# Optimization experiments

Measured on AMD Instinct MI355X. Metric: run time of the kernel, lower is better.

## Reference

```python
import jax, jax.numpy as jnp
import numpy as np

N_A = 100000   # target-type nodes
N_B = 100000   # source-type nodes
IN_DIM = 256
OUT_DIM = 256
E = 320000     # edges per meta-path
LN_EPS = 1e-5


def setup_inputs() -> dict:
    key = jax.random.key(0)
    ks = jax.random.split(key, 10)
    w_scale = 1.0 / np.sqrt(IN_DIM)
    return {
        "x_A": jax.random.normal(ks[0], (N_A, IN_DIM), jnp.float32),
        "x_B": jax.random.normal(ks[1], (N_B, IN_DIM), jnp.float32),
        "edge_index0": jax.random.randint(ks[2], (2, E), 0, N_A, dtype=jnp.int32),
        "edge_index1": jax.random.randint(ks[3], (2, E), 0, N_A, dtype=jnp.int32),
        "W0": jax.random.normal(ks[4], (IN_DIM, OUT_DIM), jnp.float32) * w_scale,
        "b0": jnp.zeros((OUT_DIM,), jnp.float32),
        "W1": jax.random.normal(ks[5], (IN_DIM, OUT_DIM), jnp.float32) * w_scale,
        "b1": jnp.zeros((OUT_DIM,), jnp.float32),
        "sem_vec": jax.random.normal(ks[6], (OUT_DIM,), jnp.float32),
        "gamma": jnp.ones((OUT_DIM,), jnp.float32),
        "beta": jnp.zeros((OUT_DIM,), jnp.float32),
    }


def _layer_norm(x, gamma, beta):
    mu = jnp.mean(x, axis=-1, keepdims=True)
    var = jnp.mean((x - mu) ** 2, axis=-1, keepdims=True)
    return (x - mu) * jax.lax.rsqrt(var + LN_EPS) * gamma + beta


def _path_mean_agg(x_src, W, b, ei, n_dst):
    # project ALL source nodes first (matches torch: proj_src = Linear(src_x))
    proj = x_src @ W + b                      # (N_src, OUT)
    msgs = proj[ei[0]]                        # gather  (E, OUT)
    agg = jax.ops.segment_sum(msgs, ei[1], num_segments=n_dst)   # scatter_add
    cnt = jax.ops.segment_sum(jnp.ones((ei.shape[1],), proj.dtype), ei[1],
                              num_segments=n_dst)
    return agg / jnp.clip(cnt, 1.0)[:, None]  # count-normalized mean


def reference(x_A, x_B, edge_index0, edge_index1, W0, b0, W1, b1,
              sem_vec, gamma, beta):
    n_dst = x_A.shape[0]
    agg0 = _path_mean_agg(x_B, W0, b0, edge_index0, n_dst)
    agg1 = _path_mean_agg(x_B, W1, b1, edge_index1, n_dst)
    stack = jnp.stack([agg0, agg1], axis=0)               # (P=2, N_A, OUT)
    scores = jnp.einsum('pnd,d->pn', jnp.tanh(stack), sem_vec)
    weights = jax.nn.softmax(scores, axis=0)              # over meta-paths
    fused = jnp.sum(stack * weights[..., None], axis=0)   # (N_A, OUT)
    out_A = _layer_norm(jax.nn.relu(fused), gamma, beta)
    out_B = jnp.zeros((x_B.shape[0], OUT_DIM), x_B.dtype)  # no path targets B
    return out_A, out_B
```

## Files before the change

kernel.cpp:

```cpp
#include <hip/hip_runtime.h>
#include <math.h>

#define NA 100000
#define NB 100000
#define KDIM 256
#define ODIM 256
#define NEDGE 320000
#define CAP 32
#define NBUCK (2 * NA)

typedef unsigned int u32;
typedef _Float16 f16x8 __attribute__((ext_vector_type(8)));
typedef float    f32x4 __attribute__((ext_vector_type(4)));

__global__ __launch_bounds__(256) void convert_w(
    const float* __restrict__ W0, const float* __restrict__ b0,
    const float* __restrict__ W1, const float* __restrict__ b1,
    _Float16* __restrict__ Wth, float* __restrict__ bcat)
{
    const int t = blockIdx.x * 256 + threadIdx.x;
    if (t >= 512 * 32) return;
    const int n  = t >> 5;
    const int kb = (t & 31) * 8;
    const float* src = (n < ODIM) ? (W0 + n) : (W1 + (n - ODIM));
    f16x8 vh;
    #pragma unroll
    for (int j = 0; j < 8; ++j)
        vh[j] = (_Float16)src[(size_t)(kb + j) * ODIM];
    *(f16x8*)&Wth[(size_t)n * KDIM + kb] = vh;
    if ((t & 31) == 0) bcat[n] = (n < ODIM) ? b0[n] : b1[n - ODIM];
}

__global__ __launch_bounds__(256) void convert_x(
    const float* __restrict__ x, _Float16* __restrict__ xh)
{
    const size_t c = ((size_t)blockIdx.x * 256 + threadIdx.x) * 8;
    const float4* p = (const float4*)&x[c];
    float4 a = p[0], b = p[1];
    f16x8 v;
    v[0] = (_Float16)a.x; v[1] = (_Float16)a.y;
    v[2] = (_Float16)a.z; v[3] = (_Float16)a.w;
    v[4] = (_Float16)b.x; v[5] = (_Float16)b.y;
    v[6] = (_Float16)b.z; v[7] = (_Float16)b.w;
    *(f16x8*)&xh[c] = v;
}

__global__ __launch_bounds__(256) void bucket_fill(
    const int* __restrict__ ei0, const int* __restrict__ ei1,
    u32* __restrict__ cnt, int* __restrict__ elist)
{
    const int gid = blockIdx.x * 256 + threadIdx.x;
    if (gid >= 2 * NEDGE) return;
    const int p = (gid >= NEDGE) ? 1 : 0;
    const int j = gid - p * NEDGE;
    const int* ei = p ? ei1 : ei0;
    const int src = ei[j];
    const int dst = ei[NEDGE + j];
    const u32 b = (u32)(p * NA + dst);
    const u32 pos = atomicAdd(&cnt[b], 1u);
    if (pos < CAP) elist[(size_t)b * CAP + pos] = src;
}

__global__ __launch_bounds__(256) void agg_mean(
    const _Float16* __restrict__ xh, const u32* __restrict__ cnt,
    const int* __restrict__ elist, _Float16* __restrict__ aggx)
{
    const int row  = (int)((blockIdx.x * (size_t)blockDim.x + threadIdx.x) >> 6);
    const int lane = threadIdx.x & 63;
    if (row >= NA) return;
    const int p  = lane >> 5;
    const int li = lane & 31;
    const int c  = li * 8;

    const u32 b  = (u32)(p * NA + row);
    const u32 nt = cnt[b];
    const u32 n  = min(nt, (u32)CAP);
    const int* el = &elist[(size_t)b * CAP];

    float a[8] = {};
    for (u32 j = 0; j < n; ++j) {
        const int src = el[j];
        const f16x8 v = *(const f16x8*)&xh[(size_t)src * KDIM + c];
        #pragma unroll
        for (int i = 0; i < 8; ++i) a[i] += (float)v[i];
    }
    const float inv = 1.0f / fmaxf((float)nt, 1.0f);
    f16x8 o;
    #pragma unroll
    for (int i = 0; i < 8; ++i) o[i] = (_Float16)(a[i] * inv);
    *(f16x8*)&aggx[((size_t)p * NA + row) * KDIM + c] = o;
}

__global__ __launch_bounds__(256) void proj_gemm(
    const _Float16* __restrict__ aggx, const _Float16* __restrict__ Wth,
    const float* __restrict__ bcat, _Float16* __restrict__ pagg)
{
    __shared__ __align__(16) char smem[17408];
    f16x8* Ah = (f16x8*)smem;
    f16x8* Bh = (f16x8*)(smem + 8192);

    const int t    = threadIdx.x;
    const int w    = t >> 6;
    const int lane = t & 63;
    const int p    = (blockIdx.y >= 782) ? 1 : 0;
    const int m0   = (blockIdx.y - p * 782) * 128;
    const int n0   = blockIdx.x * 128;
    const int wm   = w & 1, wn = w >> 1;
    const int r16  = lane & 15;
    const int kc   = (lane >> 4) * 8;
    const int srow = w * 16 + r16;

    const int arow0 = min(m0 + srow,      NA - 1);
    const int arow1 = min(m0 + srow + 64, NA - 1);
    const _Float16* Ap = aggx + (size_t)p * NA * KDIM;
    const int brow0 = p * 256 + n0 + srow;
    const int brow1 = brow0 + 64;

    f32x4 acc[4][4] = {};

    for (int k0 = 0; k0 < KDIM; k0 += 32) {
        f16x8 ga0 = *(const f16x8*)&Ap[(size_t)arow0 * KDIM + k0 + kc];
        f16x8 ga1 = *(const f16x8*)&Ap[(size_t)arow1 * KDIM + k0 + kc];
        f16x8 gh0 = *(const f16x8*)&Wth[(size_t)brow0 * KDIM + k0 + kc];
        f16x8 gh1 = *(const f16x8*)&Wth[(size_t)brow1 * KDIM + k0 + kc];

        __syncthreads();
        Ah[t] = ga0;  Ah[t + 256] = ga1;
        Bh[t] = gh0;  Bh[t + 256] = gh1;
        __syncthreads();

        f16x8 af[4], bgh[4];
        #pragma unroll
        for (int i = 0; i < 4; ++i) af[i] = Ah[(wm * 4 + i) * 64 + lane];
        #pragma unroll
        for (int j = 0; j < 4; ++j) bgh[j] = Bh[(wn * 4 + j) * 64 + lane];
        #pragma unroll
        for (int i = 0; i < 4; ++i)
            #pragma unroll
            for (int j = 0; j < 4; ++j)
                acc[i][j] = __builtin_amdgcn_mfma_f32_16x16x32_f16(
                    af[i], bgh[j], acc[i][j], 0, 0, 0);
    }

    float bias[4];
    #pragma unroll
    for (int j = 0; j < 4; ++j)
        bias[j] = bcat[p * 256 + n0 + wn * 64 + j * 16 + r16];

    const int quad = lane >> 4, c16 = lane & 15;
    const int lr = lane >> 2, lc = (lane & 3) * 16;

    for (int i = 0; i < 4; ++i) {
        __syncthreads();
        float* ep = (float*)(smem + w * 4352);
        #pragma unroll
        for (int j = 0; j < 4; ++j)
            #pragma unroll
            for (int r = 0; r < 4; ++r)
                ep[(quad * 4 + r) * 68 + j * 16 + c16] = acc[i][j][r] + bias[j];
        __syncthreads();
        f32x4 v0 = *(f32x4*)&ep[lr * 68 + lc + 0];
        f32x4 v1 = *(f32x4*)&ep[lr * 68 + lc + 4];
        f32x4 v2 = *(f32x4*)&ep[lr * 68 + lc + 8];
        f32x4 v3 = *(f32x4*)&ep[lr * 68 + lc + 12];
        const int rg = m0 + wm * 64 + i * 16 + lr;
        if (rg < NA) {
            f16x8 o0, o1;
            o0[0] = (_Float16)v0[0]; o0[1] = (_Float16)v0[1];
            o0[2] = (_Float16)v0[2]; o0[3] = (_Float16)v0[3];
            o0[4] = (_Float16)v1[0]; o0[5] = (_Float16)v1[1];
            o0[6] = (_Float16)v1[2]; o0[7] = (_Float16)v1[3];
            o1[0] = (_Float16)v2[0]; o1[1] = (_Float16)v2[1];
            o1[2] = (_Float16)v2[2]; o1[3] = (_Float16)v2[3];
            o1[4] = (_Float16)v3[0]; o1[5] = (_Float16)v3[1];
            o1[6] = (_Float16)v3[2]; o1[7] = (_Float16)v3[3];
            _Float16* dst = &pagg[((size_t)p * NA + rg) * ODIM + n0 + wn * 64 + lc];
            *(f16x8*)(dst + 0) = o0;
            *(f16x8*)(dst + 8) = o1;
        }
    }
}

__global__ __launch_bounds__(256) void finalize(
    _Float16* __restrict__ pagg, const u32* __restrict__ cnt,
    float* __restrict__ out,
    const float* __restrict__ sem, const float* __restrict__ gamma,
    const float* __restrict__ beta)
{
    const int row  = (int)((blockIdx.x * (size_t)blockDim.x + threadIdx.x) >> 6);
    const int lane = threadIdx.x & 63;
    if (row >= NA) return;
    const int p  = lane >> 5;
    const int li = lane & 31;
    const int c  = li * 8;

    const u32 n = cnt[p * NA + row];
    _Float16* pp = &pagg[((size_t)p * NA + row) * ODIM + c];
    const f16x8 v = *(const f16x8*)pp;
    float m[8];
    #pragma unroll
    for (int i = 0; i < 8; ++i) m[i] = (n > 0) ? (float)v[i] : 0.0f;

    f16x8 z = {};
    *(f16x8*)pp = z;

    float4 s0 = *(const float4*)&sem[c];
    float4 s1 = *(const float4*)&sem[c + 4];
    float sv[8] = {s0.x, s0.y, s0.z, s0.w, s1.x, s1.y, s1.z, s1.w};
    float s = 0.f;
    #pragma unroll
    for (int i = 0; i < 8; ++i) s += tanhf(m[i]) * sv[i];
    #pragma unroll
    for (int off = 1; off <= 16; off <<= 1) s += __shfl_xor(s, off);
    const float so = __shfl_xor(s, 32);
    const float mx = fmaxf(s, so);
    const float e  = __expf(s - mx), eo = __expf(so - mx);
    const float wown = e / (e + eo), woth = eo / (e + eo);

    float fused[8];
    float sum = 0.f, sq = 0.f;
    #pragma unroll
    for (int i = 0; i < 8; ++i) {
        const float mo = __shfl_xor(m[i], 32);
        float f = fmaxf(wown * m[i] + woth * mo, 0.f);
        fused[i] = f;
        sum += f;
        sq  += f * f;
    }
    #pragma unroll
    for (int off = 1; off <= 32; off <<= 1) {
        sum += __shfl_xor(sum, off);
        sq  += __shfl_xor(sq,  off);
    }
    const float mu  = sum * (0.5f / ODIM);
    const float var = sq  * (0.5f / ODIM) - mu * mu;
    const float rinv = rsqrtf(var + 1e-5f);

    if (p == 0) {
        float4 g0 = *(const float4*)&gamma[c];
        float4 g1 = *(const float4*)&gamma[c + 4];
        float4 b0 = *(const float4*)&beta[c];
        float4 b1 = *(const float4*)&beta[c + 4];
        float gv[8] = {g0.x, g0.y, g0.z, g0.w, g1.x, g1.y, g1.z, g1.w};
        float bv[8] = {b0.x, b0.y, b0.z, b0.w, b1.x, b1.y, b1.z, b1.w};
        float o[8];
        #pragma unroll
        for (int i = 0; i < 8; ++i) o[i] = (fused[i] - mu) * rinv * gv[i] + bv[i];
        float4 o0, o1;
        o0.x = o[0]; o0.y = o[1]; o0.z = o[2]; o0.w = o[3];
        o1.x = o[4]; o1.y = o[5]; o1.z = o[6]; o1.w = o[7];
        *(float4*)&out[(size_t)row * ODIM + c]     = o0;
        *(float4*)&out[(size_t)row * ODIM + c + 4] = o1;
    }
}

extern "C" void kernel_launch(void* const* d_in, const int* in_sizes, int n_in,
                              void* d_out, int out_size, void* d_ws, size_t ws_size,
                              hipStream_t stream)
{
    const float* xB   = (const float*)d_in[1];
    const int*   ei0  = (const int*)d_in[2];
    const int*   ei1  = (const int*)d_in[3];
    const float* W0   = (const float*)d_in[4];
    const float* b0   = (const float*)d_in[5];
    const float* W1   = (const float*)d_in[6];
    const float* b1   = (const float*)d_in[7];
    const float* sem  = (const float*)d_in[8];
    const float* gam  = (const float*)d_in[9];
    const float* bet  = (const float*)d_in[10];

    float* out = (float*)d_out;

    _Float16* xh   = (_Float16*)d_ws;
    _Float16* aggx = xh + (size_t)NB * KDIM;
    u32* cnt   = (u32*)(aggx + (size_t)2 * NA * KDIM);
    int* elist = (int*)(cnt + NBUCK);
    _Float16* Wth = (_Float16*)(elist + (size_t)NBUCK * CAP);
    float*    bcat = (float*)(Wth + (size_t)512 * KDIM);

    _Float16* pagg = (_Float16*)(out + (size_t)NA * ODIM);

    convert_w<<<64, 256, 0, stream>>>(W0, b0, W1, b1, Wth, bcat);

    convert_x<<<(NB * KDIM / 8) / 256, 256, 0, stream>>>(xB, xh);

    hipMemsetAsync(cnt, 0, (size_t)NBUCK * sizeof(u32), stream);
    bucket_fill<<<(2 * NEDGE + 255) / 256, 256, 0, stream>>>(ei0, ei1, cnt, elist);

    agg_mean<<<(NA + 3) / 4, 256, 0, stream>>>(xh, cnt, elist, aggx);

    proj_gemm<<<dim3(2, 1564), 256, 0, stream>>>(aggx, Wth, bcat, pagg);

    finalize<<<(NA + 3) / 4, 256, 0, stream>>>(pagg, cnt, out, sem, gam, bet);
}
```

Measured before the change: 582.6 us.

## Fuse projection GEMM with semantic-attention and LayerNorm finalize via shared memory

Merges the projection GEMM and the finalize kernel into one kernel. Each block computes a 64-row tile for both meta-paths, keeps the fp16 projected results in LDS, and runs softmax fusion and LayerNorm from there. This removes the round trip of the intermediate projected tensor through global memory (previously staged in out_B) and one launch. The same kernel now zeroes out_B directly. In exchange, B fragments are read straight from global memory rather than shared, the accumulator count per thread doubles (register pressure), and the large LDS buffer may lower occupancy.

```diff
diff --git a/kernel.cpp b/kernel.cpp
--- a/kernel.cpp
+++ b/kernel.cpp
@@ -91,166 +91,147 @@
     *(f16x8*)&aggx[((size_t)p * NA + row) * KDIM + c] = o;
 }
 
-__global__ __launch_bounds__(256) void proj_gemm(
+__global__ __launch_bounds__(256) void gemm_finalize(
     const _Float16* __restrict__ aggx, const _Float16* __restrict__ Wth,
-    const float* __restrict__ bcat, _Float16* __restrict__ pagg)
-{
-    __shared__ __align__(16) char smem[17408];
-    f16x8* Ah = (f16x8*)smem;
-    f16x8* Bh = (f16x8*)(smem + 8192);
+    const float* __restrict__ bcat, const u32* __restrict__ cnt,
+    const float* __restrict__ sem, const float* __restrict__ gamma,
+    const float* __restrict__ beta, float* __restrict__ out)
+{
+    __shared__ __align__(16) f16x8 Ah[512];
+    __shared__ __align__(16) _Float16 P[64][520];
 
     const int t    = threadIdx.x;
     const int w    = t >> 6;
     const int lane = t & 63;
-    const int p    = (blockIdx.y >= 782) ? 1 : 0;
-    const int m0   = (blockIdx.y - p * 782) * 128;
-    const int n0   = blockIdx.x * 128;
-    const int wm   = w & 1, wn = w >> 1;
+    const int m0   = blockIdx.x * 64;
+    const int p    = w >> 1;
+    const int n0w  = (w & 1) * 128;
     const int r16  = lane & 15;
     const int kc   = (lane >> 4) * 8;
     const int srow = w * 16 + r16;
 
-    const int arow0 = min(m0 + srow,      NA - 1);
-    const int arow1 = min(m0 + srow + 64, NA - 1);
-    const _Float16* Ap = aggx + (size_t)p * NA * KDIM;
-    const int brow0 = p * 256 + n0 + srow;
-    const int brow1 = brow0 + 64;
-
-    f32x4 acc[4][4] = {};
+    {
+        float* outB = out + (size_t)NA * ODIM;
+        f32x4 z = {};
+        #pragma unroll
+        for (int it = 0; it < 16; ++it) {
+            const int idx = it * 256 + t;
+            const int r = idx >> 6;
+            if (m0 + r < NA)
+                *(f32x4*)&outB[(size_t)(m0 + r) * ODIM + (idx & 63) * 4] = z;
+        }
+    }
+
+    const int arow  = min(m0 + srow, NA - 1);
+    const size_t a0off = (size_t)arow * KDIM + kc;
+    const size_t a1off = ((size_t)NA + arow) * KDIM + kc;
+
+    int boff[8];
+    #pragma unroll
+    for (int j = 0; j < 8; ++j)
+        boff[j] = (p * 256 + n0w + j * 16 + r16) * KDIM + kc;
+
+    f32x4 acc[4][8] = {};
 
     for (int k0 = 0; k0 < KDIM; k0 += 32) {
-        f16x8 ga0 = *(const f16x8*)&Ap[(size_t)arow0 * KDIM + k0 + kc];
-        f16x8 ga1 = *(const f16x8*)&Ap[(size_t)arow1 * KDIM + k0 + kc];
-        f16x8 gh0 = *(const f16x8*)&Wth[(size_t)brow0 * KDIM + k0 + kc];
-        f16x8 gh1 = *(const f16x8*)&Wth[(size_t)brow1 * KDIM + k0 + kc];
-
+        const f16x8 ga0 = *(const f16x8*)&aggx[a0off + k0];
+        const f16x8 ga1 = *(const f16x8*)&aggx[a1off + k0];
         __syncthreads();
         Ah[t] = ga0;  Ah[t + 256] = ga1;
-        Bh[t] = gh0;  Bh[t + 256] = gh1;
         __syncthreads();
 
-        f16x8 af[4], bgh[4];
-        #pragma unroll
-        for (int i = 0; i < 4; ++i) af[i] = Ah[(wm * 4 + i) * 64 + lane];
-        #pragma unroll
-        for (int j = 0; j < 4; ++j) bgh[j] = Bh[(wn * 4 + j) * 64 + lane];
-        #pragma unroll
-        for (int i = 0; i < 4; ++i)
+        f16x8 af[4];
+        #pragma unroll
+        for (int i = 0; i < 4; ++i) af[i] = Ah[p * 256 + i * 64 + lane];
+        #pragma unroll
+        for (int j = 0; j < 8; ++j) {
+            const f16x8 bh = *(const f16x8*)&Wth[boff[j] + k0];
             #pragma unroll
-            for (int j = 0; j < 4; ++j)
+            for (int i = 0; i < 4; ++i)
                 acc[i][j] = __builtin_amdgcn_mfma_f32_16x16x32_f16(
-                    af[i], bgh[j], acc[i][j], 0, 0, 0);
-    }
-
-    float bias[4];
-    #pragma unroll
-    for (int j = 0; j < 4; ++j)
-        bias[j] = bcat[p * 256 + n0 + wn * 64 + j * 16 + r16];
+                    af[i], bh, acc[i][j], 0, 0, 0);
+        }
+    }
 
     const int quad = lane >> 4, c16 = lane & 15;
-    const int lr = lane >> 2, lc = (lane & 3) * 16;
-
-    for (int i = 0; i < 4; ++i) {
-        __syncthreads();
-        float* ep = (float*)(smem + w * 4352);
-        #pragma unroll
-        for (int j = 0; j < 4; ++j)
+    float bias[8];
+    #pragma unroll
+    for (int j = 0; j < 8; ++j)
+        bias[j] = bcat[p * 256 + n0w + j * 16 + c16];
+    #pragma unroll
+    for (int i = 0; i < 4; ++i)
+        #pragma unroll
+        for (int j = 0; j < 8; ++j)
             #pragma unroll
-            for (int r = 0; r < 4; ++r)
-                ep[(quad * 4 + r) * 68 + j * 16 + c16] = acc[i][j][r] + bias[j];
-        __syncthreads();
-        f32x4 v0 = *(f32x4*)&ep[lr * 68 + lc + 0];
-        f32x4 v1 = *(f32x4*)&ep[lr * 68 + lc + 4];
-        f32x4 v2 = *(f32x4*)&ep[lr * 68 + lc + 8];
-        f32x4 v3 = *(f32x4*)&ep[lr * 68 + lc + 12];
-        const int rg = m0 + wm * 64 + i * 16 + lr;
-        if (rg < NA) {
-            f16x8 o0, o1;
-            o0[0] = (_Float16)v0[0]; o0[1] = (_Float16)v0[1];
-            o0[2] = (_Float16)v0[2]; o0[3] = (_Float16)v0[3];
-            o0[4] = (_Float16)v1[0]; o0[5] = (_Float16)v1[1];
-            o0[6] = (_Float16)v1[2]; o0[7] = (_Float16)v1[3];
-            o1[0] = (_Float16)v2[0]; o1[1] = (_Float16)v2[1];
-            o1[2] = (_Float16)v2[2]; o1[3] = (_Float16)v2[3];
-            o1[4] = (_Float16)v3[0]; o1[5] = (_Float16)v3[1];
-            o1[6] = (_Float16)v3[2]; o1[7] = (_Float16)v3[3];
-            _Float16* dst = &pagg[((size_t)p * NA + rg) * ODIM + n0 + wn * 64 + lc];
-            *(f16x8*)(dst + 0) = o0;
-            *(f16x8*)(dst + 8) = o1;
-        }
-    }
-}
-
-__global__ __launch_bounds__(256) void finalize(
-    _Float16* __restrict__ pagg, const u32* __restrict__ cnt,
-    float* __restrict__ out,
-    const float* __restrict__ sem, const float* __restrict__ gamma,
-    const float* __restrict__ beta)
-{
-    const int row  = (int)((blockIdx.x * (size_t)blockDim.x + threadIdx.x) >> 6);
-    const int lane = threadIdx.x & 63;
-    if (row >= NA) return;
-    const int p  = lane >> 5;
+            for (int e = 0; e < 4; ++e)
+                P[i * 16 + quad * 4 + e][p * 256 + n0w + j * 16 + c16] =
+                    (_Float16)(acc[i][j][e] + bias[j]);
+    __syncthreads();
+
+    const int fp = lane >> 5;
     const int li = lane & 31;
     const int c  = li * 8;
 
-    const u32 n = cnt[p * NA + row];
-    _Float16* pp = &pagg[((size_t)p * NA + row) * ODIM + c];
-    const f16x8 v = *(const f16x8*)pp;
-    float m[8];
-    #pragma unroll
-    for (int i = 0; i < 8; ++i) m[i] = (n > 0) ? (float)v[i] : 0.0f;
-
-    f16x8 z = {};
-    *(f16x8*)pp = z;
-
-    float4 s0 = *(const float4*)&sem[c];
-    float4 s1 = *(const float4*)&sem[c + 4];
-    float sv[8] = {s0.x, s0.y, s0.z, s0.w, s1.x, s1.y, s1.z, s1.w};
-    float s = 0.f;
-    #pragma unroll
-    for (int i = 0; i < 8; ++i) s += tanhf(m[i]) * sv[i];
-    #pragma unroll
-    for (int off = 1; off <= 16; off <<= 1) s += __shfl_xor(s, off);
-    const float so = __shfl_xor(s, 32);
-    const float mx = fmaxf(s, so);
-    const float e  = __expf(s - mx), eo = __expf(so - mx);
-    const float wown = e / (e + eo), woth = eo / (e + eo);
-
-    float fused[8];
-    float sum = 0.f, sq = 0.f;
-    #pragma unroll
-    for (int i = 0; i < 8; ++i) {
-        const float mo = __shfl_xor(m[i], 32);
-        float f = fmaxf(wown * m[i] + woth * mo, 0.f);
-        fused[i] = f;
-        sum += f;
-        sq  += f * f;
-    }
-    #pragma unroll
-    for (int off = 1; off <= 32; off <<= 1) {
-        sum += __shfl_xor(sum, off);
-        sq  += __shfl_xor(sq,  off);
-    }
-    const float mu  = sum * (0.5f / ODIM);
-    const float var = sq  * (0.5f / ODIM) - mu * mu;
-    const float rinv = rsqrtf(var + 1e-5f);
-
-    if (p == 0) {
-        float4 g0 = *(const float4*)&gamma[c];
-        float4 g1 = *(const float4*)&gamma[c + 4];
-        float4 b0 = *(const float4*)&beta[c];
-        float4 b1 = *(const float4*)&beta[c + 4];
-        float gv[8] = {g0.x, g0.y, g0.z, g0.w, g1.x, g1.y, g1.z, g1.w};
-        float bv[8] = {b0.x, b0.y, b0.z, b0.w, b1.x, b1.y, b1.z, b1.w};
-        float o[8];
-        #pragma unroll
-        for (int i = 0; i < 8; ++i) o[i] = (fused[i] - mu) * rinv * gv[i] + bv[i];
-        float4 o0, o1;
-        o0.x = o[0]; o0.y = o[1]; o0.z = o[2]; o0.w = o[3];
-        o1.x = o[4]; o1.y = o[5]; o1.z = o[6]; o1.w = o[7];
-        *(float4*)&out[(size_t)row * ODIM + c]     = o0;
-        *(float4*)&out[(size_t)row * ODIM + c + 4] = o1;
+    for (int rr = 0; rr < 16; ++rr) {
+        const int r  = w * 16 + rr;
+        const int rg = m0 + r;
+        if (rg >= NA) break;
+
+        const u32 n = cnt[fp * NA + rg];
+        const f16x8 v = *(const f16x8*)&P[r][fp * 256 + c];
+        float m[8];
+        #pragma unroll
+        for (int i = 0; i < 8; ++i) m[i] = (n > 0) ? (float)v[i] : 0.0f;
+
+        float4 s0 = *(const float4*)&sem[c];
+        float4 s1 = *(const float4*)&sem[c + 4];
+        float sv[8] = {s0.x, s0.y, s0.z, s0.w, s1.x, s1.y, s1.z, s1.w};
+        float s = 0.f;
+        #pragma unroll
+        for (int i = 0; i < 8; ++i) s += tanhf(m[i]) * sv[i];
+        #pragma unroll
+        for (int off = 1; off <= 16; off <<= 1) s += __shfl_xor(s, off);
+        const float so = __shfl_xor(s, 32);
+        const float mx = fmaxf(s, so);
+        const float e  = __expf(s - mx), eo = __expf(so - mx);
+        const float wown = e / (e + eo), woth = eo / (e + eo);
+
+        float fused[8];
+        float sum = 0.f, sq = 0.f;
+        #pragma unroll
+        for (int i = 0; i < 8; ++i) {
+            const float mo = __shfl_xor(m[i], 32);
+            float f = fmaxf(wown * m[i] + woth * mo, 0.f);
+            fused[i] = f;
+            sum += f;
+            sq  += f * f;
+        }
+        #pragma unroll
+        for (int off = 1; off <= 32; off <<= 1) {
+            sum += __shfl_xor(sum, off);
+            sq  += __shfl_xor(sq,  off);
+        }
+        const float mu  = sum * (0.5f / ODIM);
+        const float var = sq  * (0.5f / ODIM) - mu * mu;
+        const float rinv = rsqrtf(var + 1e-5f);
+
+        if (fp == 0) {
+            float4 g0 = *(const float4*)&gamma[c];
+            float4 g1 = *(const float4*)&gamma[c + 4];
+            float4 b0 = *(const float4*)&beta[c];
+            float4 b1 = *(const float4*)&beta[c + 4];
+            float gv[8] = {g0.x, g0.y, g0.z, g0.w, g1.x, g1.y, g1.z, g1.w};
+            float bv[8] = {b0.x, b0.y, b0.z, b0.w, b1.x, b1.y, b1.z, b1.w};
+            float o[8];
+            #pragma unroll
+            for (int i = 0; i < 8; ++i)
+                o[i] = (fused[i] - mu) * rinv * gv[i] + bv[i];
+            float4 o0, o1;
+            o0.x = o[0]; o0.y = o[1]; o0.z = o[2]; o0.w = o[3];
+            o1.x = o[4]; o1.y = o[5]; o1.z = o[6]; o1.w = o[7];
+            *(float4*)&out[(size_t)rg * ODIM + c]     = o0;
+            *(float4*)&out[(size_t)rg * ODIM + c + 4] = o1;
+        }
     }
 }
 
@@ -278,8 +259,6 @@
     _Float16* Wth = (_Float16*)(elist + (size_t)NBUCK * CAP);
     float*    bcat = (float*)(Wth + (size_t)512 * KDIM);
 
-    _Float16* pagg = (_Float16*)(out + (size_t)NA * ODIM);
-
     convert_w<<<64, 256, 0, stream>>>(W0, b0, W1, b1, Wth, bcat);
 
     convert_x<<<(NB * KDIM / 8) / 256, 256, 0, stream>>>(xB, xh);
@@ -289,7 +268,6 @@
 
     agg_mean<<<(NA + 3) / 4, 256, 0, stream>>>(xh, cnt, elist, aggx);
 
-    proj_gemm<<<dim3(2, 1564), 256, 0, stream>>>(aggx, Wth, bcat, pagg);
-
-    finalize<<<(NA + 3) / 4, 256, 0, stream>>>(pagg, cnt, out, sem, gam, bet);
-}
+    gemm_finalize<<<(NA + 63) / 64, 256, 0, stream>>>(aggx, Wth, bcat, cnt,
+                                                      sem, gam, bet, out);
+}
```

Result: slower. 659.4 us (+13.2%).

## Merge prep kernels and widen GEMM tile to full N with direct-global B loads

Applied to the files above, without the earlier changes.

Merges the W conversion, x conversion and count memset into one prep kernel, which removes two launches and a memset. The projection GEMM now gives each block all 256 output columns, so every A tile is loaded from global memory once instead of twice. B fragments are read straight from global/L2 into registers rather than staged through shared memory. This doubles the accumulator registers (4x8 f32x4) and may lower occupancy, and the uncached B loads can add latency inside the MFMA loop.

```diff
diff --git a/kernel.cpp b/kernel.cpp
--- a/kernel.cpp
+++ b/kernel.cpp
@@ -13,36 +13,40 @@
 typedef _Float16 f16x8 __attribute__((ext_vector_type(8)));
 typedef float    f32x4 __attribute__((ext_vector_type(4)));
 
-__global__ __launch_bounds__(256) void convert_w(
+__global__ __launch_bounds__(256) void prep(
     const float* __restrict__ W0, const float* __restrict__ b0,
     const float* __restrict__ W1, const float* __restrict__ b1,
-    _Float16* __restrict__ Wth, float* __restrict__ bcat)
-{
-    const int t = blockIdx.x * 256 + threadIdx.x;
-    if (t >= 512 * 32) return;
-    const int n  = t >> 5;
-    const int kb = (t & 31) * 8;
-    const float* src = (n < ODIM) ? (W0 + n) : (W1 + (n - ODIM));
-    f16x8 vh;
-    #pragma unroll
-    for (int j = 0; j < 8; ++j)
-        vh[j] = (_Float16)src[(size_t)(kb + j) * ODIM];
-    *(f16x8*)&Wth[(size_t)n * KDIM + kb] = vh;
-    if ((t & 31) == 0) bcat[n] = (n < ODIM) ? b0[n] : b1[n - ODIM];
-}
-
-__global__ __launch_bounds__(256) void convert_x(
-    const float* __restrict__ x, _Float16* __restrict__ xh)
-{
-    const size_t c = ((size_t)blockIdx.x * 256 + threadIdx.x) * 8;
-    const float4* p = (const float4*)&x[c];
-    float4 a = p[0], b = p[1];
-    f16x8 v;
-    v[0] = (_Float16)a.x; v[1] = (_Float16)a.y;
-    v[2] = (_Float16)a.z; v[3] = (_Float16)a.w;
-    v[4] = (_Float16)b.x; v[5] = (_Float16)b.y;
-    v[6] = (_Float16)b.z; v[7] = (_Float16)b.w;
-    *(f16x8*)&xh[c] = v;
+    const float* __restrict__ x,
+    _Float16* __restrict__ Wth, float* __restrict__ bcat,
+    _Float16* __restrict__ xh, u32* __restrict__ cnt)
+{
+    const int gid = blockIdx.x * 256 + threadIdx.x;
+
+    if (gid < NBUCK) cnt[gid] = 0u;
+
+    if (gid < 512 * 32) {
+        const int n  = gid >> 5;
+        const int kb = (gid & 31) * 8;
+        const float* src = (n < ODIM) ? (W0 + n) : (W1 + (n - ODIM));
+        f16x8 vh;
+        #pragma unroll
+        for (int j = 0; j < 8; ++j)
+            vh[j] = (_Float16)src[(size_t)(kb + j) * ODIM];
+        *(f16x8*)&Wth[(size_t)n * KDIM + kb] = vh;
+        if ((gid & 31) == 0) bcat[n] = (n < ODIM) ? b0[n] : b1[n - ODIM];
+    }
+
+    const size_t c = (size_t)gid * 8;
+    if (c < (size_t)NB * KDIM) {
+        const float4* p = (const float4*)&x[c];
+        float4 a = p[0], b = p[1];
+        f16x8 v;
+        v[0] = (_Float16)a.x; v[1] = (_Float16)a.y;
+        v[2] = (_Float16)a.z; v[3] = (_Float16)a.w;
+        v[4] = (_Float16)b.x; v[5] = (_Float16)b.y;
+        v[6] = (_Float16)b.z; v[7] = (_Float16)b.w;
+        *(f16x8*)&xh[c] = v;
+    }
 }
 
 __global__ __launch_bounds__(256) void bucket_fill(
@@ -97,14 +101,12 @@
 {
     __shared__ __align__(16) char smem[17408];
     f16x8* Ah = (f16x8*)smem;
-    f16x8* Bh = (f16x8*)(smem + 8192);
 
     const int t    = threadIdx.x;
     const int w    = t >> 6;
     const int lane = t & 63;
-    const int p    = (blockIdx.y >= 782) ? 1 : 0;
-    const int m0   = (blockIdx.y - p * 782) * 128;
-    const int n0   = blockIdx.x * 128;
+    const int p    = (blockIdx.x >= 782) ? 1 : 0;
+    const int m0   = (blockIdx.x - p * 782) * 128;
     const int wm   = w & 1, wn = w >> 1;
     const int r16  = lane & 15;
     const int kc   = (lane >> 4) * 8;
@@ -113,70 +115,76 @@
     const int arow0 = min(m0 + srow,      NA - 1);
     const int arow1 = min(m0 + srow + 64, NA - 1);
     const _Float16* Ap = aggx + (size_t)p * NA * KDIM;
-    const int brow0 = p * 256 + n0 + srow;
-    const int brow1 = brow0 + 64;
-
-    f32x4 acc[4][4] = {};
+
+    int boff[8];
+    #pragma unroll
+    for (int j = 0; j < 8; ++j)
+        boff[j] = (p * 256 + wn * 128 + j * 16 + r16) * KDIM + kc;
+
+    f32x4 acc[4][8] = {};
 
     for (int k0 = 0; k0 < KDIM; k0 += 32) {
-        f16x8 ga0 = *(const f16x8*)&Ap[(size_t)arow0 * KDIM + k0 + kc];
-        f16x8 ga1 = *(const f16x8*)&Ap[(size_t)arow1 * KDIM + k0 + kc];
-        f16x8 gh0 = *(const f16x8*)&Wth[(size_t)brow0 * KDIM + k0 + kc];
-        f16x8 gh1 = *(const f16x8*)&Wth[(size_t)brow1 * KDIM + k0 + kc];
-
+        const f16x8 ga0 = *(const f16x8*)&Ap[(size_t)arow0 * KDIM + k0 + kc];
+        const f16x8 ga1 = *(const f16x8*)&Ap[(size_t)arow1 * KDIM + k0 + kc];
         __syncthreads();
         Ah[t] = ga0;  Ah[t + 256] = ga1;
-        Bh[t] = gh0;  Bh[t + 256] = gh1;
         __syncthreads();
 
-        f16x8 af[4], bgh[4];
+        f16x8 af[4];
         #pragma unroll
         for (int i = 0; i < 4; ++i) af[i] = Ah[(wm * 4 + i) * 64 + lane];
         #pragma unroll
-        for (int j = 0; j < 4; ++j) bgh[j] = Bh[(wn * 4 + j) * 64 + lane];
-        #pragma unroll
-        for (int i = 0; i < 4; ++i)
+        for (int j = 0; j < 8; ++j) {
+            const f16x8 bh = *(const f16x8*)&Wth[boff[j] + k0];
             #pragma unroll
-            for (int j = 0; j < 4; ++j)
+            for (int i = 0; i < 4; ++i)
                 acc[i][j] = __builtin_amdgcn_mfma_f32_16x16x32_f16(
-                    af[i], bgh[j], acc[i][j], 0, 0, 0);
-    }
-
-    float bias[4];
-    #pragma unroll
-    for (int j = 0; j < 4; ++j)
-        bias[j] = bcat[p * 256 + n0 + wn * 64 + j * 16 + r16];
+                    af[i], bh, acc[i][j], 0, 0, 0);
+        }
+    }
+
+    float bias[8];
+    #pragma unroll
+    for (int j = 0; j < 8; ++j)
+        bias[j] = bcat[p * 256 + wn * 128 + j * 16 + r16];
 
     const int quad = lane >> 4, c16 = lane & 15;
     const int lr = lane >> 2, lc = (lane & 3) * 16;
 
     for (int i = 0; i < 4; ++i) {
-        __syncthreads();
-        float* ep = (float*)(smem + w * 4352);
-        #pragma unroll
-        for (int j = 0; j < 4; ++j)
+        #pragma unroll
+        for (int jh = 0; jh < 2; ++jh) {
+            __syncthreads();
+            float* ep = (float*)(smem + w * 4352);
             #pragma unroll
-            for (int r = 0; r < 4; ++r)
-                ep[(quad * 4 + r) * 68 + j * 16 + c16] = acc[i][j][r] + bias[j];
-        __syncthreads();
-        f32x4 v0 = *(f32x4*)&ep[lr * 68 + lc + 0];
-        f32x4 v1 = *(f32x4*)&ep[lr * 68 + lc + 4];
-        f32x4 v2 = *(f32x4*)&ep[lr * 68 + lc + 8];
-        f32x4 v3 = *(f32x4*)&ep[lr * 68 + lc + 12];
-        const int rg = m0 + wm * 64 + i * 16 + lr;
-        if (rg < NA) {
-            f16x8 o0, o1;
-            o0[0] = (_Float16)v0[0]; o0[1] = (_Float16)v0[1];
-            o0[2] = (_Float16)v0[2]; o0[3] = (_Float16)v0[3];
-            o0[4] = (_Float16)v1[0]; o0[5] = (_Float16)v1[1];
-            o0[6] = (_Float16)v1[2]; o0[7] = (_Float16)v1[3];
-            o1[0] = (_Float16)v2[0]; o1[1] = (_Float16)v2[1];
-            o1[2] = (_Float16)v2[2]; o1[3] = (_Float16)v2[3];
-            o1[4] = (_Float16)v3[0]; o1[5] = (_Float16)v3[1];
-            o1[6] = (_Float16)v3[2]; o1[7] = (_Float16)v3[3];
-            _Float16* dst = &pagg[((size_t)p * NA + rg) * ODIM + n0 + wn * 64 + lc];
-            *(f16x8*)(dst + 0) = o0;
-            *(f16x8*)(dst + 8) = o1;
+            for (int jj = 0; jj < 4; ++jj) {
+                const int j = jh * 4 + jj;
+                #pragma unroll
+                for (int r = 0; r < 4; ++r)
+                    ep[(quad * 4 + r) * 68 + jj * 16 + c16] =
+                        acc[i][j][r] + bias[j];
+            }
+            __syncthreads();
+            f32x4 v0 = *(f32x4*)&ep[lr * 68 + lc + 0];
+            f32x4 v1 = *(f32x4*)&ep[lr * 68 + lc + 4];
+            f32x4 v2 = *(f32x4*)&ep[lr * 68 + lc + 8];
+            f32x4 v3 = *(f32x4*)&ep[lr * 68 + lc + 12];
+            const int rg = m0 + wm * 64 + i * 16 + lr;
+            if (rg < NA) {
+                f16x8 o0, o1;
+                o0[0] = (_Float16)v0[0]; o0[1] = (_Float16)v0[1];
+                o0[2] = (_Float16)v0[2]; o0[3] = (_Float16)v0[3];
+                o0[4] = (_Float16)v1[0]; o0[5] = (_Float16)v1[1];
+                o0[6] = (_Float16)v1[2]; o0[7] = (_Float16)v1[3];
+                o1[0] = (_Float16)v2[0]; o1[1] = (_Float16)v2[1];
+                o1[2] = (_Float16)v2[2]; o1[3] = (_Float16)v2[3];
+                o1[4] = (_Float16)v3[0]; o1[5] = (_Float16)v3[1];
+                o1[6] = (_Float16)v3[2]; o1[7] = (_Float16)v3[3];
+                _Float16* dst = &pagg[((size_t)p * NA + rg) * ODIM
+                                      + wn * 128 + jh * 64 + lc];
+                *(f16x8*)(dst + 0) = o0;
+                *(f16x8*)(dst + 8) = o1;
+            }
         }
     }
 }
@@ -280,16 +288,14 @@
 
     _Float16* pagg = (_Float16*)(out + (size_t)NA * ODIM);
 
-    convert_w<<<64, 256, 0, stream>>>(W0, b0, W1, b1, Wth, bcat);
-
-    convert_x<<<(NB * KDIM / 8) / 256, 256, 0, stream>>>(xB, xh);
-
-    hipMemsetAsync(cnt, 0, (size_t)NBUCK * sizeof(u32), stream);
+    prep<<<(NB * KDIM / 8) / 256, 256, 0, stream>>>(W0, b0, W1, b1, xB,
+                                                    Wth, bcat, xh, cnt);
+
     bucket_fill<<<(2 * NEDGE + 255) / 256, 256, 0, stream>>>(ei0, ei1, cnt, elist);
 
     agg_mean<<<(NA + 3) / 4, 256, 0, stream>>>(xh, cnt, elist, aggx);
 
-    proj_gemm<<<dim3(2, 1564), 256, 0, stream>>>(aggx, Wth, bcat, pagg);
+    proj_gemm<<<1564, 256, 0, stream>>>(aggx, Wth, bcat, pagg);
 
     finalize<<<(NA + 3) / 4, 256, 0, stream>>>(pagg, cnt, out, sem, gam, bet);
 }
```

New measurement: 628.6 us. 7.9% more time.
